# Optimization experiments

Measured on AMD Instinct MI355X. Metric: run time of the kernel, lower is better.

Reference implementation:

```python
import jax, jax.numpy as jnp
import numpy as np

NUM_HEADS = 16

def _rope_tables(seq_len, head_dim):
    # inv_freq over even indices; freqs = outer(t, inv_freq) -> [S, head_dim//2]
    inv_freq = 1.0 / (10000.0 ** (jnp.arange(0, head_dim, 2, dtype=jnp.float32) / head_dim))
    t = jnp.arange(seq_len, dtype=jnp.float32)
    freqs = t[:, None] * inv_freq[None, :]
    return jnp.cos(freqs), jnp.sin(freqs)  # each [S, head_dim//2]

def _apply_rope(x, cos, sin):
    # x: [B,H,S,hd]; cos/sin: [S, hd//2] broadcast to [1,1,S,hd//2]
    hd = x.shape[-1]
    x1, x2 = x[..., : hd // 2], x[..., hd // 2 :]
    c = cos[None, None]
    s = sin[None, None]
    return jnp.concatenate([x1 * c - x2 * s, x2 * c + x1 * s], axis=-1)

def setup_inputs() -> dict:
    key = jax.random.key(0)
    k1, k2, k3 = jax.random.split(key, 3)
    B, S, D = 2, 2048, 1024
    x = jax.random.normal(k1, (B, S, D), dtype=jnp.float32)
    w_qkv = jax.random.normal(k2, (3 * D, D), dtype=jnp.float32) * (2.0 / D) ** 0.5
    w_out = jax.random.normal(k3, (D, D), dtype=jnp.float32) * (2.0 / D) ** 0.5
    b_out = jnp.zeros((D,), dtype=jnp.float32)
    return {"x": x, "w_qkv": w_qkv, "w_out": w_out, "b_out": b_out}

def reference(x, w_qkv, w_out, b_out):
    B, S, D = x.shape
    H = NUM_HEADS
    hd = D // H
    scale = hd ** -0.5
    qkv = jnp.einsum("bsd,ed->bse", x, w_qkv)  # [B,S,3D]
    qkv = qkv.reshape(B, S, 3, H, hd).transpose(2, 0, 3, 1, 4)  # [3,B,H,S,hd]
    q, k, v = qkv[0], qkv[1], qkv[2]
    cos, sin = _rope_tables(S, hd)
    q = _apply_rope(q, cos, sin)
    k = _apply_rope(k, cos, sin)
    scores = jnp.einsum("bhqd,bhkd->bhqk", q, k) * scale  # [B,H,S,S]
    attn = jax.nn.softmax(scores, axis=-1)
    out = jnp.einsum("bhqk,bhkd->bhqd", attn, v)  # [B,H,S,hd]
    out = out.transpose(0, 2, 1, 3).reshape(B, S, D)
    return jnp.einsum("bsd,ed->bse", out, w_out) + b_out
```

## Files before the change

### kernel.cpp

```cpp
#include <hip/hip_runtime.h>
#include <hip/hip_bf16.h>
#include <math.h>

typedef __bf16 bf16;
typedef __attribute__((ext_vector_type(8))) __bf16 bf16x8;
typedef __attribute__((ext_vector_type(4))) __bf16 bf16x4;
typedef __attribute__((ext_vector_type(4))) float f32x4;
typedef __attribute__((ext_vector_type(16))) float f32x16;

#define MFMA16(a, b, c) __builtin_amdgcn_mfma_f32_16x16x32_bf16((a), (b), (c), 0, 0, 0)
#define MFMA32(a, b, c) __builtin_amdgcn_mfma_f32_32x32x16_bf16((a), (b), (c), 0, 0, 0)

__device__ __forceinline__ float fexp2(float x) { return __builtin_amdgcn_exp2f(x); }

__device__ __forceinline__ int swz(int row, int col) {
  return row * 64 + ((((col) >> 3) ^ (row & 7)) << 3) + (col & 7);
}

__device__ __forceinline__ void gl_lds16(const bf16* g, bf16* l) {
  __builtin_amdgcn_global_load_lds(
      (const __attribute__((address_space(1))) void*)g,
      (__attribute__((address_space(3))) void*)l, 16, 0, 0);
}

__global__ __launch_bounds__(256) void cvt_all(const float* __restrict__ x,
                                               const float* __restrict__ wq,
                                               const float* __restrict__ wo,
                                               bf16* __restrict__ xb,
                                               bf16* __restrict__ wqb,
                                               bf16* __restrict__ wob) {
  int i = blockIdx.x * 256 + threadIdx.x;
  const float* src;
  bf16* dst;
  int off;
  if (i < 1048576)       { src = x;  dst = xb;  off = i; }
  else if (i < 1835008)  { src = wq; dst = wqb; off = i - 1048576; }
  else                   { src = wo; dst = wob; off = i - 1835008; }
  float4 v = ((const float4*)src)[off];
  bf16x4 o = {(bf16)v.x, (bf16)v.y, (bf16)v.z, (bf16)v.w};
  ((bf16x4*)dst)[off] = o;
}

__global__ __launch_bounds__(256) void gemm_bt(const bf16* __restrict__ A,
                                               const bf16* __restrict__ Bm,
                                               float* __restrict__ Cf,
                                               const float* __restrict__ bias,
                                               int M, int N, int K) {
  __shared__ __align__(16) bf16 As[128 * 64];
  __shared__ __align__(16) bf16 Bs[128 * 64];
  const int t = threadIdx.x;
  const int w = t >> 6, l = t & 63;
  const int wr = w >> 1, wc = w & 1;
  const int lr = l & 15, lh = l >> 4;
  const int bm = blockIdx.x * 128, bn = blockIdx.y * 128;
  const int srow = l >> 3;
  const int schunk = (l & 7) ^ srow;

  f32x4 acc[4][4] = {};

  for (int k0 = 0; k0 < K; k0 += 64) {
    __syncthreads();
#pragma unroll
    for (int jj = 0; jj < 4; ++jj) {
      const int j = w + jj * 4;
      const int r = j * 8 + srow;
      gl_lds16(A + (size_t)(bm + r) * K + k0 + schunk * 8, As + j * 512);
      gl_lds16(Bm + (size_t)(bn + r) * K + k0 + schunk * 8, Bs + j * 512);
    }
    __syncthreads();
#pragma unroll
    for (int kk = 0; kk < 2; ++kk) {
      bf16x8 af[4], bfr[4];
#pragma unroll
      for (int mt = 0; mt < 4; ++mt)
        af[mt] = *(const bf16x8*)(As + swz(wr * 64 + mt * 16 + lr, kk * 32 + lh * 8));
#pragma unroll
      for (int nt = 0; nt < 4; ++nt)
        bfr[nt] = *(const bf16x8*)(Bs + swz(wc * 64 + nt * 16 + lr, kk * 32 + lh * 8));
#pragma unroll
      for (int mt = 0; mt < 4; ++mt)
#pragma unroll
        for (int nt = 0; nt < 4; ++nt)
          acc[mt][nt] = MFMA16(af[mt], bfr[nt], acc[mt][nt]);
    }
  }

#pragma unroll
  for (int mt = 0; mt < 4; ++mt)
#pragma unroll
    for (int nt = 0; nt < 4; ++nt)
#pragma unroll
      for (int r = 0; r < 4; ++r) {
        int m = bm + wr * 64 + mt * 16 + lh * 4 + r;
        int n = bn + wc * 64 + nt * 16 + lr;
        Cf[(size_t)m * N + n] = acc[mt][nt][r] + bias[n];
      }
}

__global__ __launch_bounds__(256) void gemm_qkv_rope(const bf16* __restrict__ A,
                                                     const bf16* __restrict__ Bm,
                                                     bf16* __restrict__ Qd,
                                                     bf16* __restrict__ Kd,
                                                     bf16* __restrict__ Vtg) {
  const int K = 1024;
  __shared__ __align__(16) bf16 As[128 * 64];
  __shared__ __align__(16) bf16 Bs[128 * 64];
  const int t = threadIdx.x;
  const int w = t >> 6, l = t & 63;
  const int wr = w >> 1, wc = w & 1;
  const int lr = l & 15, lh = l >> 4;
  const int bm = blockIdx.x * 128, bn = blockIdx.y * 128;
  const int srow = l >> 3;
  const int schunk = (l & 7) ^ srow;

  f32x4 acc[4][4] = {};

  for (int k0 = 0; k0 < K; k0 += 64) {
    __syncthreads();
#pragma unroll
    for (int jj = 0; jj < 4; ++jj) {
      const int j = w + jj * 4;
      const int r = j * 8 + srow;
      gl_lds16(A + (size_t)(bm + r) * K + k0 + schunk * 8, As + j * 512);
      gl_lds16(Bm + (size_t)(bn + r) * K + k0 + schunk * 8, Bs + j * 512);
    }
    __syncthreads();
#pragma unroll
    for (int kk = 0; kk < 2; ++kk) {
      bf16x8 af[4], bfr[4];
#pragma unroll
      for (int mt = 0; mt < 4; ++mt)
        af[mt] = *(const bf16x8*)(As + swz(wr * 64 + mt * 16 + lr, kk * 32 + lh * 8));
#pragma unroll
      for (int nt = 0; nt < 4; ++nt)
        bfr[nt] = *(const bf16x8*)(Bs + swz(wc * 64 + nt * 16 + lr, kk * 32 + lh * 8));
#pragma unroll
      for (int mt = 0; mt < 4; ++mt)
#pragma unroll
        for (int nt = 0; nt < 4; ++nt)
          acc[mt][nt] = MFMA16(af[mt], bfr[nt], acc[mt][nt]);
    }
  }

  const int b = bm >> 11;
  const int sbase = (bm & 2047) + wr * 64 + lh * 4;
  const int sec = bn >> 10;
  const int h = ((bn & 1023) + wc * 64) >> 6;
  const int bh = b * 16 + h;

  if (sec < 2) {
    bf16* dst = (sec == 0 ? Qd : Kd) + (size_t)bh * 2048 * 64;
    const float QSs = sec == 0 ? 0.18033688011112042f : 1.0f;
#pragma unroll
    for (int nt = 0; nt < 2; ++nt) {
      const int j = nt * 16 + lr;
      const float ifr = fexp2((float)j * -0.4152410118609203f) *
                        0.15915494309189535f;
#pragma unroll
      for (int mt = 0; mt < 4; ++mt) {
#pragma unroll
        for (int r = 0; r < 4; ++r) {
          const int s = sbase + mt * 16 + r;
          float rev = (float)s * ifr;
          rev -= floorf(rev);
          float c  = __builtin_amdgcn_cosf(rev);
          float sn = __builtin_amdgcn_sinf(rev);
          float x1 = acc[mt][nt][r], x2 = acc[mt][nt + 2][r];
          dst[(size_t)s * 64 + j]      = (bf16)((x1 * c - x2 * sn) * QSs);
          dst[(size_t)s * 64 + j + 32] = (bf16)((x2 * c + x1 * sn) * QSs);
        }
      }
    }
  } else {
    bf16* dst = Vtg + (size_t)bh * 131072;
#pragma unroll
    for (int nt = 0; nt < 4; ++nt) {
      const int d = nt * 16 + lr;
#pragma unroll
      for (int mt = 0; mt < 4; ++mt) {
        const int g = sbase + mt * 16;
        const int gp = (g & ~12) | ((g & 4) << 1) | ((g & 8) >> 1);
        bf16x4 v4 = {(bf16)acc[mt][nt][0], (bf16)acc[mt][nt][1],
                     (bf16)acc[mt][nt][2], (bf16)acc[mt][nt][3]};
        *(bf16x4*)(dst + (size_t)d * 2048 + gp) = v4;
      }
    }
  }
}

__global__ __launch_bounds__(512) void attn_fwd(const bf16* __restrict__ Qg,
                                                const bf16* __restrict__ Kg,
                                                const bf16* __restrict__ Vtg,
                                                bf16* __restrict__ Og) {
  __shared__ __align__(16) bf16 Ks[2 * 32 * 128];
  __shared__ __align__(16) bf16 Vt[2 * 32 * 128];
  const int bh = blockIdx.x, qt = blockIdx.y;
  const int t = threadIdx.x, wv = t >> 6, l = t & 63;
  const int lq = l & 31, hi = l >> 5;
  const bf16* Qb  = Qg  + (size_t)bh * 2048 * 64;
  const bf16* Kb  = Kg  + (size_t)bh * 2048 * 64;
  const bf16* Vtb = Vtg + (size_t)bh * 131072;
  const int q = qt * 256 + wv * 32 + lq;

  bf16x8 qf[4];
#pragma unroll
  for (int s = 0; s < 4; ++s)
    qf[s] = *(const bf16x8*)(Qb + (size_t)q * 64 + s * 16 + hi * 8);

  bf16x8 onesf;
#pragma unroll
  for (int e = 0; e < 8; ++e) onesf[e] = (bf16)1.0f;

  f32x16 o0 = {}, o1 = {};
  f32x16 lacc = {};

  const int vhalf = t >> 8;
  const int ch = t & 255;
  const int r0 = ch >> 2, c0 = (ch & 3) * 16;
  const int srow = r0 & 31;
  const int L0 = ((r0 >> 5) << 3) + (c0 >> 3);
  const int off0 = srow * 128 + (((L0)     ^ (r0 & 15)) << 3);
  const int off1 = srow * 128 + (((L0 + 1) ^ (r0 & 15)) << 3);
  bf16* ldst = vhalf ? Vt : Ks;

  bf16x8 sreg[2][2];
#pragma unroll
  for (int hh = 0; hh < 2; ++hh) {
    if (vhalf) {
      sreg[hh][0] = *(const bf16x8*)(Vtb + (size_t)r0 * 2048 + hh * 64 + c0);
      sreg[hh][1] = *(const bf16x8*)(Vtb + (size_t)r0 * 2048 + hh * 64 + c0 + 8);
    } else {
      sreg[hh][0] = *(const bf16x8*)(Kb + (size_t)(hh * 64 + r0) * 64 + c0);
      sreg[hh][1] = *(const bf16x8*)(Kb + (size_t)(hh * 64 + r0) * 64 + c0 + 8);
    }
  }

  for (int tt = 0; tt < 16; ++tt) {
    __syncthreads();
#pragma unroll
    for (int hh = 0; hh < 2; ++hh) {
      *(bf16x8*)(ldst + hh * 4096 + off0) = sreg[hh][0];
      *(bf16x8*)(ldst + hh * 4096 + off1) = sreg[hh][1];
    }
    __syncthreads();

    if (tt + 1 < 16) {
      const int KV2 = (tt + 1) * 128;
#pragma unroll
      for (int hh = 0; hh < 2; ++hh) {
        if (vhalf) {
          sreg[hh][0] = *(const bf16x8*)(Vtb + (size_t)r0 * 2048 + KV2 + hh * 64 + c0);
          sreg[hh][1] = *(const bf16x8*)(Vtb + (size_t)r0 * 2048 + KV2 + hh * 64 + c0 + 8);
        } else {
          sreg[hh][0] = *(const bf16x8*)(Kb + (size_t)(KV2 + hh * 64 + r0) * 64 + c0);
          sreg[hh][1] = *(const bf16x8*)(Kb + (size_t)(KV2 + hh * 64 + r0) * 64 + c0 + 8);
        }
      }
    }

#pragma unroll
    for (int hh = 0; hh < 2; ++hh) {
      const bf16* Kp = Ks + hh * 4096;
      const bf16* Vp = Vt + hh * 4096;

      f32x16 p0 = {}, p1 = {};
      __builtin_amdgcn_s_setprio(1);
#pragma unroll
      for (int s = 0; s < 4; ++s) {
        bf16x8 ka0 = *(const bf16x8*)(Kp + lq * 128 + (((2 * s + hi) ^ (lq & 15)) << 3));
        bf16x8 ka1 = *(const bf16x8*)(Kp + lq * 128 + (((8 + 2 * s + hi) ^ (lq & 15)) << 3));
        p0 = MFMA32(ka0, qf[s], p0);
        p1 = MFMA32(ka1, qf[s], p1);
      }
      __builtin_amdgcn_s_setprio(0);

#pragma unroll
      for (int j = 0; j < 16; ++j) {
        p0[j] = fexp2(p0[j]);
        p1[j] = fexp2(p1[j]);
      }

      __builtin_amdgcn_s_setprio(1);
#pragma unroll
      for (int s = 0; s < 4; ++s) {
        bf16x8 pb;
#pragma unroll
        for (int e = 0; e < 8; ++e) {
          float pv = (s == 0) ? p0[e] : (s == 1) ? p0[8 + e]
                   : (s == 2) ? p1[e] : p1[8 + e];
          pb[e] = (bf16)pv;
        }
        bf16x8 va0 = *(const bf16x8*)(Vp + lq * 128 + (((2 * s + hi) ^ (lq & 15)) << 3));
        bf16x8 va1 = *(const bf16x8*)(Vp + lq * 128 + (((8 + 2 * s + hi) ^ (lq & 15)) << 3));
        o0 = MFMA32(va0, pb, o0);
        o1 = MFMA32(va1, pb, o1);
        lacc = MFMA32(onesf, pb, lacc);
      }
      __builtin_amdgcn_s_setprio(0);
    }
  }

  float inv = 1.0f / lacc[0];
  const int b = bh >> 4, h = bh & 15;
  bf16* orow = Og + (size_t)(b * 2048 + q) * 1024 + h * 64;
#pragma unroll
  for (int dblk = 0; dblk < 2; ++dblk) {
#pragma unroll
    for (int J = 0; J < 4; ++J) {
      float e0 = (dblk ? o1[4 * J] : o0[4 * J]) * inv;
      float e1 = (dblk ? o1[4 * J + 1] : o0[4 * J + 1]) * inv;
      float e2 = (dblk ? o1[4 * J + 2] : o0[4 * J + 2]) * inv;
      float e3 = (dblk ? o1[4 * J + 3] : o0[4 * J + 3]) * inv;
      bf16x4 wv2 = {(bf16)e0, (bf16)e1, (bf16)e2, (bf16)e3};
      *(bf16x4*)(orow + dblk * 32 + 8 * J + 4 * hi) = wv2;
    }
  }
}

extern "C" void kernel_launch(void* const* d_in, const int* in_sizes, int n_in,
                              void* d_out, int out_size, void* d_ws, size_t ws_size,
                              hipStream_t stream) {
  const float* x     = (const float*)d_in[0];
  const float* w_qkv = (const float*)d_in[1];
  const float* w_out = (const float*)d_in[2];
  const float* b_out = (const float*)d_in[3];
  float* out = (float*)d_out;
  char* ws = (char*)d_ws;
  const size_t MB = 1024 * 1024;

  bf16* xb    = (bf16*)(ws);
  bf16* wqkvb = (bf16*)(ws + 8 * MB);
  bf16* woutb = (bf16*)(ws + 14 * MB);
  bf16* Qd    = (bf16*)(ws + 40 * MB);
  bf16* Kd    = (bf16*)(ws + 48 * MB);
  bf16* Vtg   = (bf16*)(ws + 56 * MB);
  bf16* attnb = xb;

  cvt_all<<<8192, 256, 0, stream>>>(x, w_qkv, w_out, xb, wqkvb, woutb);

  gemm_qkv_rope<<<dim3(32, 24), 256, 0, stream>>>(xb, wqkvb, Qd, Kd, Vtg);
  attn_fwd<<<dim3(32, 8), 512, 0, stream>>>(Qd, Kd, Vtg, attnb);
  gemm_bt<<<dim3(32, 8), 256, 0, stream>>>(attnb, woutb, out, b_out,
                                           4096, 1024, 1024);
}
```

Measured before the change: 116.7 us.

## Double-buffer K/V tiles in LDS with one barrier per iteration

Doubles the LDS buffers for K and V^T in the attention kernel so each iteration writes the next tile into the alternate buffer while computing on the current one. The register prefetch now runs two tiles ahead. This cuts the barriers per iteration from two to one, aiming to hide global and LDS latency behind MFMA work. In exchange LDS use per block doubles to 64 KB and more registers stay live, which may lower occupancy.

```diff
diff --git a/kernel.cpp b/kernel.cpp
--- a/kernel.cpp
+++ b/kernel.cpp
@@ -192,8 +192,8 @@
                                                 const bf16* __restrict__ Kg,
                                                 const bf16* __restrict__ Vtg,
                                                 bf16* __restrict__ Og) {
-  __shared__ __align__(16) bf16 Ks[2 * 32 * 128];
-  __shared__ __align__(16) bf16 Vt[2 * 32 * 128];
+  __shared__ __align__(16) bf16 Ks[2 * 2 * 32 * 128];
+  __shared__ __align__(16) bf16 Vt[2 * 2 * 32 * 128];
   const int bh = blockIdx.x, qt = blockIdx.y;
   const int t = threadIdx.x, wv = t >> 6, l = t & 63;
   const int lq = l & 31, hi = l >> 5;
@@ -224,44 +224,46 @@
   bf16* ldst = vhalf ? Vt : Ks;
 
   bf16x8 sreg[2][2];
+#define LOAD_PAIR(pp)                                                          \
+  {                                                                            \
+    const int KVB = (pp) * 128;                                                \
+    _Pragma("unroll")                                                          \
+    for (int hh = 0; hh < 2; ++hh) {                                           \
+      if (vhalf) {                                                             \
+        sreg[hh][0] = *(const bf16x8*)(Vtb + (size_t)r0 * 2048 + KVB + hh * 64 + c0);      \
+        sreg[hh][1] = *(const bf16x8*)(Vtb + (size_t)r0 * 2048 + KVB + hh * 64 + c0 + 8);  \
+      } else {                                                                 \
+        sreg[hh][0] = *(const bf16x8*)(Kb + (size_t)(KVB + hh * 64 + r0) * 64 + c0);       \
+        sreg[hh][1] = *(const bf16x8*)(Kb + (size_t)(KVB + hh * 64 + r0) * 64 + c0 + 8);   \
+      }                                                                        \
+    }                                                                          \
+  }
+
+  LOAD_PAIR(0);
 #pragma unroll
   for (int hh = 0; hh < 2; ++hh) {
-    if (vhalf) {
-      sreg[hh][0] = *(const bf16x8*)(Vtb + (size_t)r0 * 2048 + hh * 64 + c0);
-      sreg[hh][1] = *(const bf16x8*)(Vtb + (size_t)r0 * 2048 + hh * 64 + c0 + 8);
-    } else {
-      sreg[hh][0] = *(const bf16x8*)(Kb + (size_t)(hh * 64 + r0) * 64 + c0);
-      sreg[hh][1] = *(const bf16x8*)(Kb + (size_t)(hh * 64 + r0) * 64 + c0 + 8);
-    }
-  }
+    *(bf16x8*)(ldst + hh * 4096 + off0) = sreg[hh][0];
+    *(bf16x8*)(ldst + hh * 4096 + off1) = sreg[hh][1];
+  }
+  LOAD_PAIR(1);
+  __syncthreads();
 
   for (int tt = 0; tt < 16; ++tt) {
-    __syncthreads();
+    const int cur = tt & 1;
+    if (tt + 1 < 16) {
+      bf16* wb = ldst + (cur ^ 1) * 8192;
+#pragma unroll
+      for (int hh = 0; hh < 2; ++hh) {
+        *(bf16x8*)(wb + hh * 4096 + off0) = sreg[hh][0];
+        *(bf16x8*)(wb + hh * 4096 + off1) = sreg[hh][1];
+      }
+    }
+    if (tt + 2 < 16) LOAD_PAIR(tt + 2);
+
 #pragma unroll
     for (int hh = 0; hh < 2; ++hh) {
-      *(bf16x8*)(ldst + hh * 4096 + off0) = sreg[hh][0];
-      *(bf16x8*)(ldst + hh * 4096 + off1) = sreg[hh][1];
-    }
-    __syncthreads();
-
-    if (tt + 1 < 16) {
-      const int KV2 = (tt + 1) * 128;
-#pragma unroll
-      for (int hh = 0; hh < 2; ++hh) {
-        if (vhalf) {
-          sreg[hh][0] = *(const bf16x8*)(Vtb + (size_t)r0 * 2048 + KV2 + hh * 64 + c0);
-          sreg[hh][1] = *(const bf16x8*)(Vtb + (size_t)r0 * 2048 + KV2 + hh * 64 + c0 + 8);
-        } else {
-          sreg[hh][0] = *(const bf16x8*)(Kb + (size_t)(KV2 + hh * 64 + r0) * 64 + c0);
-          sreg[hh][1] = *(const bf16x8*)(Kb + (size_t)(KV2 + hh * 64 + r0) * 64 + c0 + 8);
-        }
-      }
-    }
-
-#pragma unroll
-    for (int hh = 0; hh < 2; ++hh) {
-      const bf16* Kp = Ks + hh * 4096;
-      const bf16* Vp = Vt + hh * 4096;
+      const bf16* Kp = Ks + cur * 8192 + hh * 4096;
+      const bf16* Vp = Vt + cur * 8192 + hh * 4096;
 
       f32x16 p0 = {}, p1 = {};
       __builtin_amdgcn_s_setprio(1);
@@ -298,6 +300,8 @@
       }
       __builtin_amdgcn_s_setprio(0);
     }
+
+    __syncthreads();
   }
 
   float inv = 1.0f / lacc[0];
@@ -315,6 +319,7 @@
       *(bf16x4*)(orow + dblk * 32 + 8 * J + 4 * hi) = wv2;
     }
   }
+#undef LOAD_PAIR
 }
 
 extern "C" void kernel_launch(void* const* d_in, const int* in_sizes, int n_in,
```

Result: no change. 116.3 us (-0.4%).
